# Kernel optimization log

Measured on AMD Instinct MI355X. Metric: run time of the kernel, lower is better.

The kernel has to match this reference:

```python
import jax, jax.numpy as jnp
import numpy as np

N_NODES = 20000
N_EDGES = 320000
N_GRAPHS = 64
SEQ = 20
SCALAR = 16
EMB = 32
HID = 128
HEADS = 4
IN_DIM = SCALAR + 5 * EMB  # 176
NEG_SLOPE = 0.2


def masked_mean_embed(table, idx):
    # table: [V, EMB], idx: [N, L] with 0 = padding
    emb = table[idx]                                  # [N, L, EMB]
    mask = (idx != 0).astype(emb.dtype)[..., None]    # [N, L, 1]
    return (emb * mask).sum(axis=1) / (mask.sum(axis=1) + 1e-9)


def gat_conv(x, src, dst, W, att_src, att_dst, bias, heads, out_ch):
    # PyG GATConv (add_self_loops already applied to src/dst), concat heads.
    N = x.shape[0]
    xw = (x @ W).reshape(N, heads, out_ch)            # [N, H, C]
    a_src = (xw * att_src).sum(-1)                    # [N, H]
    a_dst = (xw * att_dst).sum(-1)                    # [N, H]
    e = jax.nn.leaky_relu(a_src[src] + a_dst[dst], NEG_SLOPE)  # [E, H]
    e_max = jax.ops.segment_max(e, dst, num_segments=N)
    e_max = jnp.where(jnp.isfinite(e_max), e_max, 0.0)
    ex = jnp.exp(e - e_max[dst])                      # [E, H]
    denom = jax.ops.segment_sum(ex, dst, num_segments=N)
    alpha = ex / (denom[dst] + 1e-16)                 # [E, H]
    msg = xw[src] * alpha[:, :, None]                 # [E, H, C]
    out = jax.ops.segment_sum(msg, dst, num_segments=N)
    return out.reshape(N, heads * out_ch) + bias


def setup_inputs() -> dict:
    key = jax.random.key(0)
    ks = jax.random.split(key, 24)
    s = 0.05
    inp = {
        "x_scalar": jax.random.normal(ks[0], (N_NODES, SCALAR), jnp.float32),
        "x_opcode": jax.random.randint(ks[1], (N_NODES, SEQ), 0, 256),
        "x_source": jax.random.randint(ks[2], (N_NODES, SEQ), 0, 512),
        "x_sink": jax.random.randint(ks[3], (N_NODES, SEQ), 0, 512),
        "x_string_manip": jax.random.randint(ks[4], (N_NODES, SEQ), 0, 128),
        "x_payload": jax.random.randint(ks[5], (N_NODES, SEQ), 0, 1024),
        "edge_index": jax.random.randint(ks[6], (2, N_EDGES), 0, N_NODES),
        "batch": jnp.sort(jax.random.randint(ks[7], (N_NODES,), 0, N_GRAPHS)),
        # embedding tables (row 0 = padding; masked out anyway)
        "emb_opcode": jax.random.normal(ks[8], (256, EMB)) * s,
        "emb_source": jax.random.normal(ks[9], (512, EMB)) * s,
        "emb_sink": jax.random.normal(ks[10], (512, EMB)) * s,
        "emb_string": jax.random.normal(ks[11], (128, EMB)) * s,
        "emb_payload": jax.random.normal(ks[12], (1024, EMB)) * s,
        "ln_gamma": jnp.ones((IN_DIM,), jnp.float32),
        "ln_beta": jnp.zeros((IN_DIM,), jnp.float32),
        "W1": jax.random.normal(ks[13], (IN_DIM, HEADS * HID)) * s,
        "att_src1": jax.random.normal(ks[14], (HEADS, HID)) * s,
        "att_dst1": jax.random.normal(ks[15], (HEADS, HID)) * s,
        "b1": jnp.zeros((HEADS * HID,), jnp.float32),
        "W2": jax.random.normal(ks[16], (HEADS * HID, HID)) * s,
        "att_src2": jax.random.normal(ks[17], (1, HID)) * s,
        "att_dst2": jax.random.normal(ks[18], (1, HID)) * s,
        "b2": jnp.zeros((HID,), jnp.float32),
        "cls_w1": jax.random.normal(ks[19], (HID, HID // 2)) * s,
        "cls_b1": jnp.zeros((HID // 2,), jnp.float32),
        "cls_w2": jax.random.normal(ks[20], (HID // 2, 2)) * s,
        "cls_b2": jnp.zeros((2,), jnp.float32),
    }
    return inp


def reference(x_scalar, x_opcode, x_source, x_sink, x_string_manip, x_payload,
              edge_index, batch,
              emb_opcode, emb_source, emb_sink, emb_string, emb_payload,
              ln_gamma, ln_beta,
              W1, att_src1, att_dst1, b1,
              W2, att_src2, att_dst2, b2,
              cls_w1, cls_b1, cls_w2, cls_b2):
    feats = jnp.concatenate([
        x_scalar,
        masked_mean_embed(emb_opcode, x_opcode),
        masked_mean_embed(emb_source, x_source),
        masked_mean_embed(emb_sink, x_sink),
        masked_mean_embed(emb_string, x_string_manip),
        masked_mean_embed(emb_payload, x_payload),
    ], axis=1)  # [N, 176]
    mu = feats.mean(-1, keepdims=True)
    var = ((feats - mu) ** 2).mean(-1, keepdims=True)
    h = (feats - mu) / jnp.sqrt(var + 1e-5) * ln_gamma + ln_beta

    # add self loops (PyG GATConv default)
    loops = jnp.arange(N_NODES, dtype=edge_index.dtype)
    src = jnp.concatenate([edge_index[0], loops])
    dst = jnp.concatenate([edge_index[1], loops])

    x = jax.nn.elu(gat_conv(h, src, dst, W1, att_src1, att_dst1, b1, HEADS, HID))
    x = jax.nn.elu(gat_conv(x, src, dst, W2, att_src2, att_dst2, b2, 1, HID))

    pooled = jax.ops.segment_max(x, batch, num_segments=N_GRAPHS)  # [G, HID]
    hcls = jax.nn.relu(pooled @ cls_w1 + cls_b1)
    return hcls @ cls_w2 + cls_b2  # [G, 2]
```

## Files before the change

### kernel.cpp

```cpp
#include <hip/hip_runtime.h>
#include <hip/hip_bf16.h>
#include <math.h>

#define N_NODES 20000
#define N_EDGES 320000
#define N_GRAPHS 64
#define SEQ 20
#define SCALAR 16
#define EMB 32
#define HID 128
#define IN_DIM 176
#define TOT_EDGES (N_EDGES + N_NODES)
#define CHUNK_SMALL 10000
#define POOL_SLICES 32

typedef _Float16 half8v __attribute__((ext_vector_type(8)));
typedef float f32x4 __attribute__((ext_vector_type(4)));
#define LO_SCALE 2048.0f
#define LO_INV (1.0f / 2048.0f)

#define PB2_ELEMS (16 * 8 * 64 * 8)
#define PB1_ELEMS (4 * 6 * 8 * 64 * 8)

__device__ inline float readlane_f(float v, int l) {
  return __uint_as_float(__builtin_amdgcn_readlane(__float_as_uint(v), l));
}
__device__ inline int readlane_i(int v, int l) {
  return __builtin_amdgcn_readlane(v, l);
}
__device__ inline float leaky(float e) { return e >= 0.f ? e : 0.2f * e; }
__device__ inline float elu(float v) { return v > 0.f ? v : expf(v) - 1.f; }

__global__ __launch_bounds__(256) void setup_kernel(
    const float* __restrict__ W1, const float* __restrict__ att_s1,
    const float* __restrict__ att_d1, const float* __restrict__ W2,
    float* __restrict__ was4, float* __restrict__ wad4,
    _Float16* __restrict__ PB1h, _Float16* __restrict__ PB1l,
    _Float16* __restrict__ PB2h, _Float16* __restrict__ PB2l) {
  int b = blockIdx.x;
  if (b < 44) {
    int lane = threadIdx.x & 63;
    int k = b * 4 + (threadIdx.x >> 6);
    if (k >= IN_DIM) return;
    const float* wrow = W1 + (size_t)k * 512;
    float s[4], d[4];
#pragma unroll
    for (int hh = 0; hh < 4; ++hh) {
      float w0 = wrow[hh * 128 + lane], w1 = wrow[hh * 128 + 64 + lane];
      float a0 = att_s1[hh * 128 + lane], a1 = att_s1[hh * 128 + 64 + lane];
      float c0 = att_d1[hh * 128 + lane], c1 = att_d1[hh * 128 + 64 + lane];
      s[hh] = w0 * a0 + w1 * a1;
      d[hh] = w0 * c0 + w1 * c1;
    }
    for (int off = 1; off < 64; off <<= 1) {
#pragma unroll
      for (int hh = 0; hh < 4; ++hh) {
        s[hh] += __shfl_xor(s[hh], off);
        d[hh] += __shfl_xor(d[hh], off);
      }
    }
    if (lane == 0) {
      *(float4*)&was4[k * 4] = make_float4(s[0], s[1], s[2], s[3]);
      *(float4*)&wad4[k * 4] = make_float4(d[0], d[1], d[2], d[3]);
    }
  } else if (b < 92) {
    int t = (b - 44) * 256 + threadIdx.x;
    int lane = t & 63, wi = t >> 6;
    int r = lane & 15, g = lane >> 4;
    int ntile = wi & 7, rem = wi >> 3;
    int ks = rem % 6, hh = rem / 6;
    int col = hh * 128 + ntile * 16 + r;
    size_t o = ((size_t)wi * 64 + lane) * 8;
#pragma unroll
    for (int j = 0; j < 8; ++j) {
      int k = ks * 32 + g * 8 + j;
      float v = (k < IN_DIM) ? W1[(size_t)k * 512 + col] : 0.f;
      _Float16 h = (_Float16)v;
      PB1h[o + j] = h;
      PB1l[o + j] = (_Float16)((v - (float)h) * LO_SCALE);
    }
  } else {
    int t = (b - 92) * 256 + threadIdx.x;
    int lane = t & 63, wi = t >> 6;
    int r = lane & 15, g = lane >> 4;
    int ks = wi >> 3, ntile = wi & 7;
    int col = ntile * 16 + r;
    size_t o = ((size_t)wi * 64 + lane) * 8;
#pragma unroll
    for (int j = 0; j < 8; ++j) {
      int k = ks * 32 + g * 8 + j;
      float v = W2[(size_t)k * 128 + col];
      _Float16 h = (_Float16)v;
      PB2h[o + j] = h;
      PB2l[o + j] = (_Float16)((v - (float)h) * LO_SCALE);
    }
  }
}

__global__ __launch_bounds__(256) void feats_ln_kernel(
    const float* __restrict__ xs,
    const int* __restrict__ i0, const int* __restrict__ i1,
    const int* __restrict__ i2, const int* __restrict__ i3,
    const int* __restrict__ i4,
    const float* __restrict__ t0, const float* __restrict__ t1,
    const float* __restrict__ t2, const float* __restrict__ t3,
    const float* __restrict__ t4,
    const float* __restrict__ gamma, const float* __restrict__ beta,
    const float* __restrict__ was4, const float* __restrict__ wad4,
    float* __restrict__ hout, float* __restrict__ a_s,
    float* __restrict__ a_d) {
  int lane = threadIdx.x & 63;
  int w = threadIdx.x >> 6;
  int n = blockIdx.x * 4 + w;
  if (n >= N_NODES) return;
  __shared__ int sidx[4][100];
  {
    int j = lane;
    int tab = j / 20, l = j - tab * 20;
    const int* ip = tab == 0 ? i0 : tab == 1 ? i1 : tab == 2 ? i2 : i3;
    sidx[w][j] = ip[n * SEQ + l];
    if (lane < 36) {
      int j2 = 64 + lane;
      int tab2 = j2 / 20, l2 = j2 - tab2 * 20;
      const int* ip2 = tab2 == 3 ? i3 : i4;
      sidx[w][j2] = ip2[n * SEQ + l2];
    }
  }
  bool l48 = lane < 48;
  float f0, f1, f2 = 0.f;
  if (lane < SCALAR) {
    f0 = xs[n * SCALAR + lane];
  } else {
    int tt = lane - SCALAR, tab = tt >> 5, d = tt & 31;
    const float* tp = tab == 0 ? t0 : t1;
    float sum = 0.f, cnt = 0.f;
#pragma unroll
    for (int l = 0; l < SEQ; ++l) {
      int id = sidx[w][tab * 20 + l];
      if (id != 0) { sum += tp[id * EMB + d]; cnt += 1.f; }
    }
    f0 = sum / (cnt + 1e-9f);
  }
  {
    int tt = 48 + lane, tab = tt >> 5, d = tt & 31;
    const float* tp = tab == 1 ? t1 : tab == 2 ? t2 : t3;
    float sum = 0.f, cnt = 0.f;
#pragma unroll
    for (int l = 0; l < SEQ; ++l) {
      int id = sidx[w][tab * 20 + l];
      if (id != 0) { sum += tp[id * EMB + d]; cnt += 1.f; }
    }
    f1 = sum / (cnt + 1e-9f);
  }
  if (l48) {
    int tt = 112 + lane, tab = tt >> 5, d = tt & 31;
    const float* tp = tab == 3 ? t3 : t4;
    float sum = 0.f, cnt = 0.f;
#pragma unroll
    for (int l = 0; l < SEQ; ++l) {
      int id = sidx[w][tab * 20 + l];
      if (id != 0) { sum += tp[id * EMB + d]; cnt += 1.f; }
    }
    f2 = sum / (cnt + 1e-9f);
  }
  float s = f0 + f1 + f2;
  for (int off = 1; off < 64; off <<= 1) s += __shfl_xor(s, off);
  float mu = s / (float)IN_DIM;
  float v = (f0 - mu) * (f0 - mu) + (f1 - mu) * (f1 - mu) +
            (l48 ? (f2 - mu) * (f2 - mu) : 0.f);
  for (int off = 1; off < 64; off <<= 1) v += __shfl_xor(v, off);
  float rstd = 1.0f / sqrtf(v / (float)IN_DIM + 1e-5f);
  float hv0 = (f0 - mu) * rstd * gamma[lane] + beta[lane];
  float hv1 = (f1 - mu) * rstd * gamma[64 + lane] + beta[64 + lane];
  float hv2 = l48 ? (f2 - mu) * rstd * gamma[128 + lane] + beta[128 + lane] : 0.f;
  float* hr = hout + (size_t)n * IN_DIM;
  hr[lane] = hv0;
  hr[64 + lane] = hv1;
  if (l48) hr[128 + lane] = hv2;

  const float4* wsv = (const float4*)was4;
  const float4* wdv = (const float4*)wad4;
  float4 wsa = wsv[lane], wsb = wsv[64 + lane];
  float4 wsc = l48 ? wsv[128 + lane] : make_float4(0.f, 0.f, 0.f, 0.f);
  float4 wda = wdv[lane], wdb = wdv[64 + lane];
  float4 wdc = l48 ? wdv[128 + lane] : make_float4(0.f, 0.f, 0.f, 0.f);
  float ps0 = hv0 * wsa.x + hv1 * wsb.x + hv2 * wsc.x;
  float ps1 = hv0 * wsa.y + hv1 * wsb.y + hv2 * wsc.y;
  float ps2 = hv0 * wsa.z + hv1 * wsb.z + hv2 * wsc.z;
  float ps3 = hv0 * wsa.w + hv1 * wsb.w + hv2 * wsc.w;
  float pd0 = hv0 * wda.x + hv1 * wdb.x + hv2 * wdc.x;
  float pd1 = hv0 * wda.y + hv1 * wdb.y + hv2 * wdc.y;
  float pd2 = hv0 * wda.z + hv1 * wdb.z + hv2 * wdc.z;
  float pd3 = hv0 * wda.w + hv1 * wdb.w + hv2 * wdc.w;
  for (int off = 1; off < 64; off <<= 1) {
    ps0 += __shfl_xor(ps0, off); ps1 += __shfl_xor(ps1, off);
    ps2 += __shfl_xor(ps2, off); ps3 += __shfl_xor(ps3, off);
    pd0 += __shfl_xor(pd0, off); pd1 += __shfl_xor(pd1, off);
    pd2 += __shfl_xor(pd2, off); pd3 += __shfl_xor(pd3, off);
  }
  if (lane == 0) {
    *(float4*)&a_s[n * 4] = make_float4(ps0, ps1, ps2, ps3);
    *(float4*)&a_d[n * 4] = make_float4(pd0, pd1, pd2, pd3);
  }
}

__global__ void count_kernel(const int* __restrict__ edge_index,
                             int* __restrict__ cnt, int E, int N) {
  int i = blockIdx.x * blockDim.x + threadIdx.x;
  if (i < E) {
    atomicAdd(&cnt[edge_index[E + i]], 1);
  } else if (i < E + N) {
    atomicAdd(&cnt[i - E], 1);
  }
}

__global__ __launch_bounds__(1024) void prefix_kernel(const int* __restrict__ cnt,
                                                      int* __restrict__ indptr,
                                                      int n, int total) {
  __shared__ int ss[1024];
  int t = threadIdx.x;
  int per = (n + 1023) / 1024;
  int beg = t * per, end = min(beg + per, n);
  int s = 0;
  for (int i = beg; i < end; ++i) s += cnt[i];
  ss[t] = s;
  __syncthreads();
  for (int off = 1; off < 1024; off <<= 1) {
    int v = (t >= off) ? ss[t - off] : 0;
    __syncthreads();
    ss[t] += v;
    __syncthreads();
  }
  int run = ss[t] - s;
  for (int i = beg; i < end; ++i) { indptr[i] = run; run += cnt[i]; }
  if (t == 0) indptr[n] = total;
}

__global__ void scatter_kernel(const int* __restrict__ edge_index,
                               const int* __restrict__ indptr,
                               int* __restrict__ cursor,
                               int* __restrict__ srcs, int E, int N) {
  int i = blockIdx.x * blockDim.x + threadIdx.x;
  int s, d;
  if (i < E) { s = edge_index[i]; d = edge_index[E + i]; }
  else if (i < E + N) { s = i - E; d = s; }
  else return;
  int pos = indptr[d] + atomicAdd(&cursor[d], 1);
  srcs[pos] = s;
}

__global__ __launch_bounds__(256) void agg1h_kernel(
    const float* __restrict__ h, const float* __restrict__ a_src,
    const float* __restrict__ a_dst, const int* __restrict__ indptr,
    const int* __restrict__ srcs, float* __restrict__ aggh,
    int n0, int nM) {
  int lane = threadIdx.x & 63;
  int ln = blockIdx.x * 4 + (threadIdx.x >> 6);
  if (ln >= nM) return;
  int n = n0 + ln;
  int beg = indptr[n], end = indptr[n + 1];
  int deg = end - beg;
  float4 ad = *(const float4*)&a_dst[n * 4];
  bool l48 = lane < 48;
  float acc[4][3] = {};

  auto body = [&](int s, float al0, float al1, float al2, float al3) {
    const float* r = h + (size_t)s * IN_DIM;
    float v0 = r[lane];
    float v1 = r[64 + lane];
    float v2 = l48 ? r[128 + lane] : 0.f;
    acc[0][0] += al0 * v0; acc[0][1] += al0 * v1; acc[0][2] += al0 * v2;
    acc[1][0] += al1 * v0; acc[1][1] += al1 * v1; acc[1][2] += al1 * v2;
    acc[2][0] += al2 * v0; acc[2][1] += al2 * v1; acc[2][2] += al2 * v2;
    acc[3][0] += al3 * v0; acc[3][1] += al3 * v1; acc[3][2] += al3 * v2;
  };

  if (deg <= 64) {
    int j = beg + lane;
    int s = 0;
    float e0 = -INFINITY, e1 = -INFINITY, e2 = -INFINITY, e3 = -INFINITY;
    if (j < end) {
      s = srcs[j];
      float4 as = *(const float4*)&a_src[s * 4];
      e0 = leaky(as.x + ad.x); e1 = leaky(as.y + ad.y);
      e2 = leaky(as.z + ad.z); e3 = leaky(as.w + ad.w);
    }
    float m0 = e0, m1 = e1, m2 = e2, m3 = e3;
    for (int off = 1; off < 64; off <<= 1) {
      m0 = fmaxf(m0, __shfl_xor(m0, off)); m1 = fmaxf(m1, __shfl_xor(m1, off));
      m2 = fmaxf(m2, __shfl_xor(m2, off)); m3 = fmaxf(m3, __shfl_xor(m3, off));
    }
    float x0 = (j < end) ? expf(e0 - m0) : 0.f;
    float x1 = (j < end) ? expf(e1 - m1) : 0.f;
    float x2 = (j < end) ? expf(e2 - m2) : 0.f;
    float x3 = (j < end) ? expf(e3 - m3) : 0.f;
    float d0 = x0, d1 = x1, d2 = x2, d3 = x3;
    for (int off = 1; off < 64; off <<= 1) {
      d0 += __shfl_xor(d0, off); d1 += __shfl_xor(d1, off);
      d2 += __shfl_xor(d2, off); d3 += __shfl_xor(d3, off);
    }
    float al0 = x0 / (d0 + 1e-16f), al1 = x1 / (d1 + 1e-16f);
    float al2 = x2 / (d2 + 1e-16f), al3 = x3 / (d3 + 1e-16f);
    int jj = 0;
    for (; jj + 2 <= deg; jj += 2) {
      int sa = readlane_i(s, jj), sb = readlane_i(s, jj + 1);
      float a0 = readlane_f(al0, jj), a1 = readlane_f(al1, jj);
      float a2 = readlane_f(al2, jj), a3 = readlane_f(al3, jj);
      float b0 = readlane_f(al0, jj + 1), b1 = readlane_f(al1, jj + 1);
      float b2 = readlane_f(al2, jj + 1), b3 = readlane_f(al3, jj + 1);
      body(sa, a0, a1, a2, a3);
      body(sb, b0, b1, b2, b3);
    }
    if (jj < deg) {
      int sa = readlane_i(s, jj);
      body(sa, readlane_f(al0, jj), readlane_f(al1, jj),
           readlane_f(al2, jj), readlane_f(al3, jj));
    }
  } else {
    float m0 = -INFINITY, m1 = -INFINITY, m2 = -INFINITY, m3 = -INFINITY;
    for (int j0 = beg; j0 < end; j0 += 64) {
      int j = j0 + lane;
      if (j < end) {
        int s = srcs[j];
        float4 as = *(const float4*)&a_src[s * 4];
        m0 = fmaxf(m0, leaky(as.x + ad.x)); m1 = fmaxf(m1, leaky(as.y + ad.y));
        m2 = fmaxf(m2, leaky(as.z + ad.z)); m3 = fmaxf(m3, leaky(as.w + ad.w));
      }
    }
    for (int off = 1; off < 64; off <<= 1) {
      m0 = fmaxf(m0, __shfl_xor(m0, off)); m1 = fmaxf(m1, __shfl_xor(m1, off));
      m2 = fmaxf(m2, __shfl_xor(m2, off)); m3 = fmaxf(m3, __shfl_xor(m3, off));
    }
    float d0 = 0.f, d1 = 0.f, d2 = 0.f, d3 = 0.f;
    for (int j0 = beg; j0 < end; j0 += 64) {
      int j = j0 + lane;
      if (j < end) {
        int s = srcs[j];
        float4 as = *(const float4*)&a_src[s * 4];
        d0 += expf(leaky(as.x + ad.x) - m0); d1 += expf(leaky(as.y + ad.y) - m1);
        d2 += expf(leaky(as.z + ad.z) - m2); d3 += expf(leaky(as.w + ad.w) - m3);
      }
    }
    for (int off = 1; off < 64; off <<= 1) {
      d0 += __shfl_xor(d0, off); d1 += __shfl_xor(d1, off);
      d2 += __shfl_xor(d2, off); d3 += __shfl_xor(d3, off);
    }
    float r0 = 1.f / (d0 + 1e-16f), r1 = 1.f / (d1 + 1e-16f);
    float r2 = 1.f / (d2 + 1e-16f), r3 = 1.f / (d3 + 1e-16f);
    for (int j0 = beg; j0 < end; j0 += 64) {
      int jn = min(64, end - j0);
      int j = j0 + lane;
      int s = 0;
      float al0 = 0.f, al1 = 0.f, al2 = 0.f, al3 = 0.f;
      if (j < end) {
        s = srcs[j];
        float4 as = *(const float4*)&a_src[s * 4];
        al0 = expf(leaky(as.x + ad.x) - m0) * r0;
        al1 = expf(leaky(as.y + ad.y) - m1) * r1;
        al2 = expf(leaky(as.z + ad.z) - m2) * r2;
        al3 = expf(leaky(as.w + ad.w) - m3) * r3;
      }
      for (int jj = 0; jj < jn; ++jj) {
        body(readlane_i(s, jj), readlane_f(al0, jj), readlane_f(al1, jj),
             readlane_f(al2, jj), readlane_f(al3, jj));
      }
    }
  }

  size_t base = (size_t)ln * (4 * IN_DIM);
#pragma unroll
  for (int hh = 0; hh < 4; ++hh) {
    aggh[base + hh * IN_DIM + lane] = acc[hh][0];
    aggh[base + hh * IN_DIM + 64 + lane] = acc[hh][1];
    if (l48) aggh[base + hh * IN_DIM + 128 + lane] = acc[hh][2];
  }
}

__global__ __launch_bounds__(256) void gemm_head_mfma_kernel(
    const float* __restrict__ aggh, const half8v* __restrict__ PBh,
    const half8v* __restrict__ PBl, const float* __restrict__ b1,
    float* __restrict__ out1, int M, int n0) {
  int lane = threadIdx.x & 63;
  int wid = (blockIdx.x * 256 + threadIdx.x) >> 6;
  int colhalf = wid & 1;
  int hh = (wid >> 1) & 3;
  int rg = wid >> 3;
  int rows0 = rg * 16;
  if (rows0 >= M) return;
  int r = lane & 15, g = lane >> 4;
  f32x4 acc[4] = {};
  f32x4 accm[4] = {};
  const float* a0 = aggh + ((size_t)(rows0 + r) * 4 + hh) * IN_DIM;
#pragma unroll 2
  for (int ks = 0; ks < 6; ++ks) {
    int kg = ks * 32 + g * 8;
    int koff = (kg + 8 <= IN_DIM) ? kg : 0;
    const float* ap = a0 + koff;
    float av[8];
    *(float4*)&av[0] = *(const float4*)(ap);
    *(float4*)&av[4] = *(const float4*)(ap + 4);
    half8v ah, al;
#pragma unroll
    for (int j = 0; j < 8; ++j) {
      _Float16 hv = (_Float16)av[j];
      ah[j] = hv;
      al[j] = (_Float16)((av[j] - (float)hv) * LO_SCALE);
    }
    const half8v* bh = PBh + (size_t)(((hh * 6 + ks) * 8 + colhalf * 4) * 64) + lane;
    const half8v* bl = PBl + (size_t)(((hh * 6 + ks) * 8 + colhalf * 4) * 64) + lane;
#pragma unroll
    for (int nt = 0; nt < 4; ++nt) {
      half8v bhv = bh[nt * 64], blv = bl[nt * 64];
      accm[nt] = __builtin_amdgcn_mfma_f32_16x16x32_f16(al, bhv, accm[nt], 0, 0, 0);
      accm[nt] = __builtin_amdgcn_mfma_f32_16x16x32_f16(ah, blv, accm[nt], 0, 0, 0);
      acc[nt]  = __builtin_amdgcn_mfma_f32_16x16x32_f16(ah, bhv, acc[nt], 0, 0, 0);
    }
  }
#pragma unroll
  for (int nt = 0; nt < 4; ++nt) {
    int col = hh * 128 + colhalf * 64 + nt * 16 + r;
    float bb = b1[col];
#pragma unroll
    for (int i = 0; i < 4; ++i) {
      int row = rows0 + g * 4 + i;
      if (row < M)
        out1[(size_t)(n0 + row) * 512 + col] =
            elu(acc[nt][i] + accm[nt][i] * LO_INV + bb);
    }
  }
}

__global__ __launch_bounds__(256) void gemm2att_mfma_kernel(
    const float* __restrict__ A, const half8v* __restrict__ PBh,
    const half8v* __restrict__ PBl, const float* __restrict__ att_s,
    const float* __restrict__ att_d, float* __restrict__ C,
    float* __restrict__ a_s, float* __restrict__ a_d, int M) {
  int lane = threadIdx.x & 63;
  int wid = (blockIdx.x * 256 + threadIdx.x) >> 6;
  int colq = wid & 3;
  int rg = wid >> 2;
  int row0 = rg * 16;
  if (row0 >= M) return;
  int r = lane & 15, g = lane >> 4;
  const float* arow = A + (size_t)(row0 + r) * 512 + g * 8;
  f32x4 acc[2] = {};
  f32x4 accm[2] = {};
#pragma unroll 2
  for (int ks = 0; ks < 16; ++ks) {
    float av[8];
    *(float4*)&av[0] = *(const float4*)(arow + ks * 32);
    *(float4*)&av[4] = *(const float4*)(arow + ks * 32 + 4);
    half8v ah, al;
#pragma unroll
    for (int j = 0; j < 8; ++j) {
      _Float16 hv = (_Float16)av[j];
      ah[j] = hv;
      al[j] = (_Float16)((av[j] - (float)hv) * LO_SCALE);
    }
    const half8v* bh = PBh + (size_t)((ks * 8 + colq * 2) * 64) + lane;
    const half8v* bl = PBl + (size_t)((ks * 8 + colq * 2) * 64) + lane;
#pragma unroll
    for (int nt = 0; nt < 2; ++nt) {
      half8v bhv = bh[nt * 64], blv = bl[nt * 64];
      accm[nt] = __builtin_amdgcn_mfma_f32_16x16x32_f16(al, bhv, accm[nt], 0, 0, 0);
      accm[nt] = __builtin_amdgcn_mfma_f32_16x16x32_f16(ah, blv, accm[nt], 0, 0, 0);
      acc[nt]  = __builtin_amdgcn_mfma_f32_16x16x32_f16(ah, bhv, acc[nt], 0, 0, 0);
    }
  }
  float ps[4] = {0.f, 0.f, 0.f, 0.f}, pd[4] = {0.f, 0.f, 0.f, 0.f};
#pragma unroll
  for (int nt = 0; nt < 2; ++nt) {
    int col = colq * 32 + nt * 16 + r;
    float as_ = att_s[col], ad_ = att_d[col];
#pragma unroll
    for (int i = 0; i < 4; ++i) {
      float v = acc[nt][i] + accm[nt][i] * LO_INV;
      int row = row0 + g * 4 + i;
      C[(size_t)row * 128 + col] = v;
      ps[i] += v * as_;
      pd[i] += v * ad_;
    }
  }
#pragma unroll
  for (int i = 0; i < 4; ++i) {
    for (int off = 1; off < 16; off <<= 1) {
      ps[i] += __shfl_xor(ps[i], off);
      pd[i] += __shfl_xor(pd[i], off);
    }
  }
  if (r == 0) {
#pragma unroll
    for (int i = 0; i < 4; ++i) {
      atomicAdd(&a_s[row0 + g * 4 + i], ps[i]);
      atomicAdd(&a_d[row0 + g * 4 + i], pd[i]);
    }
  }
}

__global__ __launch_bounds__(256) void agg2_kernel(
    const float* __restrict__ xw, const float* __restrict__ a_src,
    const float* __restrict__ a_dst, const int* __restrict__ indptr,
    const int* __restrict__ srcs, const float* __restrict__ bias,
    float* __restrict__ out) {
  int lane = threadIdx.x & 63;
  int n = blockIdx.x * 4 + (threadIdx.x >> 6);
  if (n >= N_NODES) return;
  int beg = indptr[n], end = indptr[n + 1];
  int deg = end - beg;
  float adn = a_dst[n];
  int half = lane >> 5, l32 = lane & 31;
  float4 acc = make_float4(0.f, 0.f, 0.f, 0.f);

  auto pairs = [&](int s, float al, int jn) {
    int jj = 0;
    for (; jj + 2 <= jn; jj += 2) {
      int sa = readlane_i(s, jj), sb = readlane_i(s, jj + 1);
      float aa = readlane_f(al, jj), ab = readlane_f(al, jj + 1);
      int sh = half ? sb : sa;
      float ahx = half ? ab : aa;
      float4 v = *(const float4*)&xw[(size_t)sh * HID + l32 * 4];
      acc.x += ahx * v.x; acc.y += ahx * v.y; acc.z += ahx * v.z; acc.w += ahx * v.w;
    }
    if (jj < jn) {
      int sa = readlane_i(s, jj);
      float ahx = half ? 0.f : readlane_f(al, jj);
      float4 v = *(const float4*)&xw[(size_t)sa * HID + l32 * 4];
      acc.x += ahx * v.x; acc.y += ahx * v.y; acc.z += ahx * v.z; acc.w += ahx * v.w;
    }
  };

  if (deg <= 64) {
    int j = beg + lane;
    int s = 0;
    float e = -INFINITY;
    if (j < end) { s = srcs[j]; e = leaky(a_src[s] + adn); }
    float m = e;
    for (int off = 1; off < 64; off <<= 1) m = fmaxf(m, __shfl_xor(m, off));
    float x = (j < end) ? expf(e - m) : 0.f;
    float d = x;
    for (int off = 1; off < 64; off <<= 1) d += __shfl_xor(d, off);
    float al = x / (d + 1e-16f);
    pairs(s, al, deg);
  } else {
    float m = -INFINITY;
    for (int j0 = beg; j0 < end; j0 += 64) {
      int j = j0 + lane;
      if (j < end) m = fmaxf(m, leaky(a_src[srcs[j]] + adn));
    }
    for (int off = 1; off < 64; off <<= 1) m = fmaxf(m, __shfl_xor(m, off));
    float d = 0.f;
    for (int j0 = beg; j0 < end; j0 += 64) {
      int j = j0 + lane;
      if (j < end) d += expf(leaky(a_src[srcs[j]] + adn) - m);
    }
    for (int off = 1; off < 64; off <<= 1) d += __shfl_xor(d, off);
    float rd = 1.f / (d + 1e-16f);
    for (int j0 = beg; j0 < end; j0 += 64) {
      int jn = min(64, end - j0);
      int j = j0 + lane;
      int s = 0;
      float al = 0.f;
      if (j < end) {
        s = srcs[j];
        al = expf(leaky(a_src[s] + adn) - m) * rd;
      }
      pairs(s, al, jn);
    }
  }

  acc.x += __shfl_xor(acc.x, 32); acc.y += __shfl_xor(acc.y, 32);
  acc.z += __shfl_xor(acc.z, 32); acc.w += __shfl_xor(acc.w, 32);
  if (half == 0) {
    float4 b = *(const float4*)&bias[l32 * 4];
    float4 o;
    o.x = elu(acc.x + b.x); o.y = elu(acc.y + b.y);
    o.z = elu(acc.z + b.z); o.w = elu(acc.w + b.w);
    *(float4*)&out[(size_t)n * HID + l32 * 4] = o;
  }
}

__global__ void gstart_kernel(const int* __restrict__ batch,
                              int* __restrict__ gstarts, int N, int G) {
  int t = threadIdx.x;
  if (t > G) return;
  int lo = 0, hi = N;
  while (lo < hi) {
    int mid = (lo + hi) >> 1;
    if (batch[mid] < t) lo = mid + 1; else hi = mid;
  }
  gstarts[t] = lo;
}

__global__ __launch_bounds__(HID) void pool_part_kernel(
    const float* __restrict__ out2, const int* __restrict__ gstarts,
    float* __restrict__ part) {
  int g = blockIdx.x, s = blockIdx.y, t = threadIdx.x;
  int beg = gstarts[g], end = gstarts[g + 1];
  int len = end - beg;
  int b0 = beg + (int)(((long long)len * s) / POOL_SLICES);
  int b1 = beg + (int)(((long long)len * (s + 1)) / POOL_SLICES);
  float m = -INFINITY;
  for (int n = b0; n < b1; ++n) m = fmaxf(m, out2[(size_t)n * HID + t]);
  part[((size_t)g * POOL_SLICES + s) * HID + t] = m;
}

__global__ __launch_bounds__(HID) void pool_reduce_kernel(
    const float* __restrict__ part, float* __restrict__ pooled) {
  int g = blockIdx.x, t = threadIdx.x;
  float m = -INFINITY;
#pragma unroll
  for (int s = 0; s < POOL_SLICES; ++s)
    m = fmaxf(m, part[((size_t)g * POOL_SLICES + s) * HID + t]);
  pooled[g * HID + t] = m;
}

__global__ __launch_bounds__(HID) void cls_kernel(const float* __restrict__ pooled,
                                                  const float* __restrict__ w1,
                                                  const float* __restrict__ b1,
                                                  const float* __restrict__ w2,
                                                  const float* __restrict__ b2,
                                                  float* __restrict__ out) {
  int g = blockIdx.x, t = threadIdx.x;
  __shared__ float sp[HID], sh1[HID / 2];
  sp[t] = pooled[g * HID + t];
  __syncthreads();
  if (t < HID / 2) {
    float s = b1[t];
    for (int k = 0; k < HID; ++k) s += sp[k] * w1[k * (HID / 2) + t];
    sh1[t] = fmaxf(s, 0.f);
  }
  __syncthreads();
  if (t < 2) {
    float o = b2[t];
    for (int k = 0; k < HID / 2; ++k) o += sh1[k] * w2[k * 2 + t];
    out[g * 2 + t] = o;
  }
}

extern "C" void kernel_launch(void* const* d_in, const int* in_sizes, int n_in,
                              void* d_out, int out_size, void* d_ws, size_t ws_size,
                              hipStream_t stream) {
  const float* x_scalar = (const float*)d_in[0];
  const int* x_opcode   = (const int*)d_in[1];
  const int* x_source   = (const int*)d_in[2];
  const int* x_sink     = (const int*)d_in[3];
  const int* x_string   = (const int*)d_in[4];
  const int* x_payload  = (const int*)d_in[5];
  const int* edge_index = (const int*)d_in[6];
  const int* batch      = (const int*)d_in[7];
  const float* emb_opcode = (const float*)d_in[8];
  const float* emb_source = (const float*)d_in[9];
  const float* emb_sink   = (const float*)d_in[10];
  const float* emb_string = (const float*)d_in[11];
  const float* emb_payload= (const float*)d_in[12];
  const float* ln_gamma = (const float*)d_in[13];
  const float* ln_beta  = (const float*)d_in[14];
  const float* W1       = (const float*)d_in[15];
  const float* att_src1 = (const float*)d_in[16];
  const float* att_dst1 = (const float*)d_in[17];
  const float* b1       = (const float*)d_in[18];
  const float* W2       = (const float*)d_in[19];
  const float* att_src2 = (const float*)d_in[20];
  const float* att_dst2 = (const float*)d_in[21];
  const float* b2       = (const float*)d_in[22];
  const float* cls_w1   = (const float*)d_in[23];
  const float* cls_b1   = (const float*)d_in[24];
  const float* cls_w2   = (const float*)d_in[25];
  const float* cls_b2   = (const float*)d_in[26];

  auto total_bytes = [&](int chunk) -> size_t {
    size_t f = (size_t)N_NODES * IN_DIM + (size_t)chunk * 4 * IN_DIM +
               (size_t)N_NODES * 512 + (size_t)N_NODES * HID +
               N_NODES * 4 * 2 + N_NODES * 2 + IN_DIM * 4 * 2 + N_GRAPHS * HID;
    size_t ii = (N_NODES + 1) + N_NODES * 2 + TOT_EDGES + (N_GRAPHS + 1);
    size_t f16b = (size_t)2 * (PB2_ELEMS + PB1_ELEMS) * sizeof(_Float16) + 32;
    size_t poolb = (size_t)N_GRAPHS * POOL_SLICES * HID * 4 + 32;
    return f * 4 + ii * 4 + f16b + poolb + 256;
  };
  int chunk = (ws_size >= total_bytes(N_NODES)) ? N_NODES : CHUNK_SMALL;

  float* h      = (float*)d_ws;
  float* aggh   = h + (size_t)N_NODES * IN_DIM;
  float* out1   = aggh + (size_t)chunk * 4 * IN_DIM;
  float* out2   = out1 + (size_t)N_NODES * 512;
  float* a1s    = out2 + (size_t)N_NODES * HID;
  float* a1d    = a1s + N_NODES * 4;
  float* was4   = a1d + N_NODES * 4;
  float* wad4   = was4 + IN_DIM * 4;
  float* pooled = wad4 + IN_DIM * 4;
  int* indptr = (int*)(pooled + N_GRAPHS * HID);
  int* cnt    = indptr + (N_NODES + 1);
  int* cursor = cnt + N_NODES;
  float* a2s  = (float*)(cursor + N_NODES);
  float* a2d  = a2s + N_NODES;
  int* srcs   = (int*)(a2d + N_NODES);
  int* gstarts= srcs + TOT_EDGES;
  uintptr_t pal = ((uintptr_t)(gstarts + N_GRAPHS + 1) + 15) & ~(uintptr_t)15;
  _Float16* PB2h = (_Float16*)pal;
  _Float16* PB2l = PB2h + PB2_ELEMS;
  _Float16* PB1h = PB2l + PB2_ELEMS;
  _Float16* PB1l = PB1h + PB1_ELEMS;
  uintptr_t ppal = ((uintptr_t)(PB1l + PB1_ELEMS) + 15) & ~(uintptr_t)15;
  float* pool_part = (float*)ppal;
  float* xw2  = h;

  hipMemsetAsync(cnt, 0, 4 * N_NODES * sizeof(int), stream);

  const int NB4 = (N_NODES + 3) / 4;

  setup_kernel<<<124, 256, 0, stream>>>(W1, att_src1, att_dst1, W2,
                                        was4, wad4, PB1h, PB1l, PB2h, PB2l);

  feats_ln_kernel<<<NB4, 256, 0, stream>>>(
      x_scalar, x_opcode, x_source, x_sink, x_string, x_payload,
      emb_opcode, emb_source, emb_sink, emb_string, emb_payload,
      ln_gamma, ln_beta, was4, wad4, h, a1s, a1d);

  int nthreads = TOT_EDGES;
  count_kernel<<<(nthreads + 255) / 256, 256, 0, stream>>>(edge_index, cnt, N_EDGES, N_NODES);
  prefix_kernel<<<1, 1024, 0, stream>>>(cnt, indptr, N_NODES, TOT_EDGES);
  scatter_kernel<<<(nthreads + 255) / 256, 256, 0, stream>>>(edge_index, indptr, cursor, srcs, N_EDGES, N_NODES);

  for (int n0 = 0; n0 < N_NODES; n0 += chunk) {
    int nM = min(chunk, N_NODES - n0);
    agg1h_kernel<<<(nM + 3) / 4, 256, 0, stream>>>(h, a1s, a1d, indptr, srcs, aggh, n0, nM);
    int rgs = (nM + 15) / 16;
    gemm_head_mfma_kernel<<<rgs * 2, 256, 0, stream>>>(
        aggh, (const half8v*)PB1h, (const half8v*)PB1l, b1, out1, nM, n0);
  }

  gemm2att_mfma_kernel<<<(N_NODES + 15) / 16, 256, 0, stream>>>(
      out1, (const half8v*)PB2h, (const half8v*)PB2l, att_src2, att_dst2,
      xw2, a2s, a2d, N_NODES);

  agg2_kernel<<<NB4, 256, 0, stream>>>(xw2, a2s, a2d, indptr, srcs, b2, out2);

  gstart_kernel<<<1, 128, 0, stream>>>(batch, gstarts, N_NODES, N_GRAPHS);
  pool_part_kernel<<<dim3(N_GRAPHS, POOL_SLICES), HID, 0, stream>>>(out2, gstarts, pool_part);
  pool_reduce_kernel<<<N_GRAPHS, HID, 0, stream>>>(pool_part, pooled);
  cls_kernel<<<N_GRAPHS, HID, 0, stream>>>(pooled, cls_w1, cls_b1, cls_w2, cls_b2, (float*)d_out);
}
```

Baseline: 382.0 us.

## Merge setup, count, gstart and scatter/feats into fewer launches

Folds the edge degree count and the graph-start binary search into the weight setup kernel as extra block ranges. It also merges the CSR scatter with the feature/LayerNorm kernel, again by splitting on block index. This cuts the preprocessing launches from six to three, removing launch overhead and the serialization between small independent kernels. In exchange, feats now waits behind the prefix scan, and the scatter's atomics share the GPU with the heavier feature work.

```diff
diff --git a/kernel.cpp b/kernel.cpp
--- a/kernel.cpp
+++ b/kernel.cpp
@@ -22,6 +22,10 @@
 #define PB2_ELEMS (16 * 8 * 64 * 8)
 #define PB1_ELEMS (4 * 6 * 8 * 64 * 8)
 
+#define SETUP_BLOCKS 124
+#define COUNT_BLOCKS ((TOT_EDGES + 255) / 256)
+#define NB4 ((N_NODES + 3) / 4)
+
 __device__ inline float readlane_f(float v, int l) {
   return __uint_as_float(__builtin_amdgcn_readlane(__float_as_uint(v), l));
 }
@@ -31,12 +35,14 @@
 __device__ inline float leaky(float e) { return e >= 0.f ? e : 0.2f * e; }
 __device__ inline float elu(float v) { return v > 0.f ? v : expf(v) - 1.f; }
 
-__global__ __launch_bounds__(256) void setup_kernel(
+__global__ __launch_bounds__(256) void setup_count_kernel(
     const float* __restrict__ W1, const float* __restrict__ att_s1,
     const float* __restrict__ att_d1, const float* __restrict__ W2,
+    const int* __restrict__ edge_index, const int* __restrict__ batch,
     float* __restrict__ was4, float* __restrict__ wad4,
     _Float16* __restrict__ PB1h, _Float16* __restrict__ PB1l,
-    _Float16* __restrict__ PB2h, _Float16* __restrict__ PB2l) {
+    _Float16* __restrict__ PB2h, _Float16* __restrict__ PB2l,
+    int* __restrict__ cnt, int* __restrict__ gstarts) {
   int b = blockIdx.x;
   if (b < 44) {
     int lane = threadIdx.x & 63;
@@ -79,7 +85,7 @@
       PB1h[o + j] = h;
       PB1l[o + j] = (_Float16)((v - (float)h) * LO_SCALE);
     }
-  } else {
+  } else if (b < SETUP_BLOCKS) {
     int t = (b - 92) * 256 + threadIdx.x;
     int lane = t & 63, wi = t >> 6;
     int r = lane & 15, g = lane >> 4;
@@ -94,10 +100,50 @@
       PB2h[o + j] = h;
       PB2l[o + j] = (_Float16)((v - (float)h) * LO_SCALE);
     }
-  }
-}
-
-__global__ __launch_bounds__(256) void feats_ln_kernel(
+  } else if (b < SETUP_BLOCKS + COUNT_BLOCKS) {
+    int i = (b - SETUP_BLOCKS) * 256 + threadIdx.x;
+    if (i < N_EDGES) {
+      atomicAdd(&cnt[edge_index[N_EDGES + i]], 1);
+    } else if (i < TOT_EDGES) {
+      atomicAdd(&cnt[i - N_EDGES], 1);
+    }
+  } else {
+    int t = threadIdx.x;
+    if (t > N_GRAPHS) return;
+    int lo = 0, hi = N_NODES;
+    while (lo < hi) {
+      int mid = (lo + hi) >> 1;
+      if (batch[mid] < t) lo = mid + 1; else hi = mid;
+    }
+    gstarts[t] = lo;
+  }
+}
+
+__global__ __launch_bounds__(1024) void prefix_kernel(const int* __restrict__ cnt,
+                                                      int* __restrict__ indptr,
+                                                      int n, int total) {
+  __shared__ int ss[1024];
+  int t = threadIdx.x;
+  int per = (n + 1023) / 1024;
+  int beg = t * per, end = min(beg + per, n);
+  int s = 0;
+  for (int i = beg; i < end; ++i) s += cnt[i];
+  ss[t] = s;
+  __syncthreads();
+  for (int off = 1; off < 1024; off <<= 1) {
+    int v = (t >= off) ? ss[t - off] : 0;
+    __syncthreads();
+    ss[t] += v;
+    __syncthreads();
+  }
+  int run = ss[t] - s;
+  for (int i = beg; i < end; ++i) { indptr[i] = run; run += cnt[i]; }
+  if (t == 0) indptr[n] = total;
+}
+
+__global__ __launch_bounds__(256) void scatter_feats_kernel(
+    const int* __restrict__ edge_index, const int* __restrict__ indptr,
+    int* __restrict__ cursor, int* __restrict__ srcs,
     const float* __restrict__ xs,
     const int* __restrict__ i0, const int* __restrict__ i1,
     const int* __restrict__ i2, const int* __restrict__ i3,
@@ -109,9 +155,20 @@
     const float* __restrict__ was4, const float* __restrict__ wad4,
     float* __restrict__ hout, float* __restrict__ a_s,
     float* __restrict__ a_d) {
+  int b = blockIdx.x;
+  if (b < COUNT_BLOCKS) {
+    int i = b * 256 + threadIdx.x;
+    int s, d;
+    if (i < N_EDGES) { s = edge_index[i]; d = edge_index[N_EDGES + i]; }
+    else if (i < TOT_EDGES) { s = i - N_EDGES; d = s; }
+    else return;
+    int pos = indptr[d] + atomicAdd(&cursor[d], 1);
+    srcs[pos] = s;
+    return;
+  }
   int lane = threadIdx.x & 63;
   int w = threadIdx.x >> 6;
-  int n = blockIdx.x * 4 + w;
+  int n = (b - COUNT_BLOCKS) * 4 + w;
   if (n >= N_NODES) return;
   __shared__ int sidx[4][100];
   {
@@ -202,51 +259,6 @@
     *(float4*)&a_s[n * 4] = make_float4(ps0, ps1, ps2, ps3);
     *(float4*)&a_d[n * 4] = make_float4(pd0, pd1, pd2, pd3);
   }
-}
-
-__global__ void count_kernel(const int* __restrict__ edge_index,
-                             int* __restrict__ cnt, int E, int N) {
-  int i = blockIdx.x * blockDim.x + threadIdx.x;
-  if (i < E) {
-    atomicAdd(&cnt[edge_index[E + i]], 1);
-  } else if (i < E + N) {
-    atomicAdd(&cnt[i - E], 1);
-  }
-}
-
-__global__ __launch_bounds__(1024) void prefix_kernel(const int* __restrict__ cnt,
-                                                      int* __restrict__ indptr,
-                                                      int n, int total) {
-  __shared__ int ss[1024];
-  int t = threadIdx.x;
-  int per = (n + 1023) / 1024;
-  int beg = t * per, end = min(beg + per, n);
-  int s = 0;
-  for (int i = beg; i < end; ++i) s += cnt[i];
-  ss[t] = s;
-  __syncthreads();
-  for (int off = 1; off < 1024; off <<= 1) {
-    int v = (t >= off) ? ss[t - off] : 0;
-    __syncthreads();
-    ss[t] += v;
-    __syncthreads();
-  }
-  int run = ss[t] - s;
-  for (int i = beg; i < end; ++i) { indptr[i] = run; run += cnt[i]; }
-  if (t == 0) indptr[n] = total;
-}
-
-__global__ void scatter_kernel(const int* __restrict__ edge_index,
-                               const int* __restrict__ indptr,
-                               int* __restrict__ cursor,
-                               int* __restrict__ srcs, int E, int N) {
-  int i = blockIdx.x * blockDim.x + threadIdx.x;
-  int s, d;
-  if (i < E) { s = edge_index[i]; d = edge_index[E + i]; }
-  else if (i < E + N) { s = i - E; d = s; }
-  else return;
-  int pos = indptr[d] + atomicAdd(&cursor[d], 1);
-  srcs[pos] = s;
 }
 
 __global__ __launch_bounds__(256) void agg1h_kernel(
@@ -577,18 +589,6 @@
     o.z = elu(acc.z + b.z); o.w = elu(acc.w + b.w);
     *(float4*)&out[(size_t)n * HID + l32 * 4] = o;
   }
-}
-
-__global__ void gstart_kernel(const int* __restrict__ batch,
-                              int* __restrict__ gstarts, int N, int G) {
-  int t = threadIdx.x;
-  if (t > G) return;
-  int lo = 0, hi = N;
-  while (lo < hi) {
-    int mid = (lo + hi) >> 1;
-    if (batch[mid] < t) lo = mid + 1; else hi = mid;
-  }
-  gstarts[t] = lo;
 }
 
 __global__ __launch_bounds__(HID) void pool_part_kernel(
@@ -706,20 +706,17 @@
 
   hipMemsetAsync(cnt, 0, 4 * N_NODES * sizeof(int), stream);
 
-  const int NB4 = (N_NODES + 3) / 4;
-
-  setup_kernel<<<124, 256, 0, stream>>>(W1, att_src1, att_dst1, W2,
-                                        was4, wad4, PB1h, PB1l, PB2h, PB2l);
-
-  feats_ln_kernel<<<NB4, 256, 0, stream>>>(
+  setup_count_kernel<<<SETUP_BLOCKS + COUNT_BLOCKS + 1, 256, 0, stream>>>(
+      W1, att_src1, att_dst1, W2, edge_index, batch,
+      was4, wad4, PB1h, PB1l, PB2h, PB2l, cnt, gstarts);
+
+  prefix_kernel<<<1, 1024, 0, stream>>>(cnt, indptr, N_NODES, TOT_EDGES);
+
+  scatter_feats_kernel<<<COUNT_BLOCKS + NB4, 256, 0, stream>>>(
+      edge_index, indptr, cursor, srcs,
       x_scalar, x_opcode, x_source, x_sink, x_string, x_payload,
       emb_opcode, emb_source, emb_sink, emb_string, emb_payload,
       ln_gamma, ln_beta, was4, wad4, h, a1s, a1d);
-
-  int nthreads = TOT_EDGES;
-  count_kernel<<<(nthreads + 255) / 256, 256, 0, stream>>>(edge_index, cnt, N_EDGES, N_NODES);
-  prefix_kernel<<<1, 1024, 0, stream>>>(cnt, indptr, N_NODES, TOT_EDGES);
-  scatter_kernel<<<(nthreads + 255) / 256, 256, 0, stream>>>(edge_index, indptr, cursor, srcs, N_EDGES, N_NODES);
 
   for (int n0 = 0; n0 < N_NODES; n0 += chunk) {
     int nM = min(chunk, N_NODES - n0);
@@ -735,7 +732,6 @@
 
   agg2_kernel<<<NB4, 256, 0, stream>>>(xw2, a2s, a2d, indptr, srcs, b2, out2);
 
-  gstart_kernel<<<1, 128, 0, stream>>>(batch, gstarts, N_NODES, N_GRAPHS);
   pool_part_kernel<<<dim3(N_GRAPHS, POOL_SLICES), HID, 0, stream>>>(out2, gstarts, pool_part);
   pool_reduce_kernel<<<N_GRAPHS, HID, 0, stream>>>(pool_part, pooled);
   cls_kernel<<<N_GRAPHS, HID, 0, stream>>>(pooled, cls_w1, cls_b1, cls_w2, cls_b2, (float*)d_out);
```

After: 368.0 us. -3.7%, faster.
